# Kernel optimization log

Measured on AMD Instinct MI355X. Metric: run time of the kernel, lower is better.

The kernel has to match this reference:

```python
import jax, jax.numpy as jnp
from jax import lax
import numpy as np

B, N, NF, EF, MD = 16, 128, 9, 3, 5
H, D, FF, L, O = 24, 768, 3072, 12, 128
NA, NID, NOD, NE, NS, NED = 4608, 256, 256, 1536, 512, 128
S = N + 1
EPS = 1e-5


def setup_inputs() -> dict:
    key = jax.random.key(0)
    ks = iter(jax.random.split(key, 64))
    emb_s = 0.02
    lin_s = 0.02 / np.sqrt(L)

    def nrm(shape, s):
        return jax.random.normal(next(ks), shape, jnp.float32) * s

    inp = {
        'x': jax.random.randint(next(ks), (B, N, NF), 0, NA + 1),
        'in_degree': jax.random.randint(next(ks), (B, N), 0, NID),
        'out_degree': jax.random.randint(next(ks), (B, N), 0, NOD),
        'spatial_pos': jax.random.randint(next(ks), (B, N, N), 0, NS),
        'edge_input': jax.random.randint(next(ks), (B, N, N, MD, EF), 0, NE + 1),
        'attn_bias': jnp.zeros((B, S, S), jnp.float32),
        # embeddings (padding_idx=0 rows zeroed)
        'atom_emb': nrm((NA + 1, D), emb_s).at[0].set(0.0),
        'in_deg_emb': nrm((NID, D), emb_s).at[0].set(0.0),
        'out_deg_emb': nrm((NOD, D), emb_s).at[0].set(0.0),
        'graph_token': nrm((1, D), emb_s),
        'edge_emb': nrm((NE + 1, H), emb_s).at[0].set(0.0),
        'edge_dis_emb': nrm((NED, H, H), emb_s),
        'spatial_emb': nrm((NS, H), emb_s).at[0].set(0.0),
        'virt_dist': nrm((1, H), emb_s),
        # stacked per-layer params
        'ln1_g': jnp.ones((L, D)), 'ln1_b': jnp.zeros((L, D)),
        'wq': nrm((L, D, D), lin_s), 'bq': jnp.zeros((L, D)),
        'wk': nrm((L, D, D), lin_s), 'bk': jnp.zeros((L, D)),
        'wv': nrm((L, D, D), lin_s), 'bv': jnp.zeros((L, D)),
        'wo': nrm((L, D, D), lin_s), 'bo': jnp.zeros((L, D)),
        'ln2_g': jnp.ones((L, D)), 'ln2_b': jnp.zeros((L, D)),
        'w1': nrm((L, D, FF), lin_s), 'b1': jnp.zeros((L, FF)),
        'w2': nrm((L, FF, D), lin_s), 'b2': jnp.zeros((L, D)),
        'final_g': jnp.ones((D,)), 'final_b': jnp.zeros((D,)),
        'out_w': nrm((D, O), lin_s), 'out_b': jnp.zeros((O,)),
    }
    return inp


def _ln(v, g, b):
    m = v.mean(-1, keepdims=True)
    va = ((v - m) ** 2).mean(-1, keepdims=True)
    return (v - m) / jnp.sqrt(va + EPS) * g + b


def _forward(x, in_degree, out_degree, spatial_pos, edge_input, attn_bias,
             atom_emb, in_deg_emb, out_deg_emb, graph_token,
             edge_emb, edge_dis_emb, spatial_emb, virt_dist,
             ln1_g, ln1_b, wq, bq, wk, bk, wv, bv, wo, bo,
             ln2_g, ln2_b, w1, b1, w2, b2, final_g, final_b, out_w, out_b):
    nb = x.shape[0]
    # ---- graph attn bias ----
    # spatial bias [B,H,N,N]
    sp_bias = spatial_emb[spatial_pos].transpose(0, 3, 1, 2)
    # multi-hop edge bias
    sp_ = jnp.where(spatial_pos == 0, 1, spatial_pos)
    sp_ = jnp.where(sp_ > 1, sp_ - 1, sp_)
    sp_ = jnp.clip(sp_, 0, MD)
    ei = edge_emb[edge_input].mean(-2)                       # [B,N,N,MD,H]
    eo = jnp.einsum('bijdh,dhk->bijk', ei, edge_dis_emb[:MD])
    edge_bias = (eo / sp_[..., None].astype(jnp.float32)).transpose(0, 3, 1, 2)
    t = virt_dist.reshape(1, H, 1)                           # virtual-token distance
    gab = jnp.repeat(attn_bias[:, None], H, axis=1)          # [B,H,S,S]
    gab = gab.at[:, :, 1:, 1:].add(sp_bias + edge_bias)
    gab = gab.at[:, :, 1:, 0].add(t)
    gab = gab.at[:, :, 0, :].add(t)
    gab = gab + attn_bias[:, None]
    # ---- node features ----
    nf = atom_emb[x].sum(-2) + in_deg_emb[in_degree] + out_deg_emb[out_degree]
    h = jnp.concatenate([jnp.broadcast_to(graph_token[None], (nb, 1, D)), nf], axis=1)  # [B,S,D]
    dk = D // H
    scale = dk ** -0.5

    def step(hc, p):
        (g1, b1n, Wq, Bq, Wk, Bk, Wv, Bv, Wo, Bo, g2, b2n, W1, B1, W2, B2) = p
        y = _ln(hc, g1, b1n)
        q = (y @ Wq + Bq).reshape(nb, S, H, dk).transpose(0, 2, 1, 3) * scale
        k = (y @ Wk + Bk).reshape(nb, S, H, dk).transpose(0, 2, 1, 3)
        v = (y @ Wv + Bv).reshape(nb, S, H, dk).transpose(0, 2, 1, 3)
        att = jnp.einsum('bhqd,bhkd->bhqk', q, k) + gab
        att = jax.nn.softmax(att, axis=-1)
        ctx = jnp.einsum('bhqk,bhkd->bhqd', att, v)
        ctx = ctx.transpose(0, 2, 1, 3).reshape(nb, S, D)
        hc = hc + (ctx @ Wo + Bo)
        y = _ln(hc, g2, b2n)
        y = jax.nn.gelu(y @ W1 + B1, approximate=False) @ W2 + B2
        return hc + y, None

    h, _ = lax.scan(step, h, (ln1_g, ln1_b, wq, bq, wk, bk, wv, bv, wo, bo,
                              ln2_g, ln2_b, w1, b1, w2, b2))
    h = _ln(h, final_g, final_b)
    return h[:, 0] @ out_w + out_b  # [B,O]


def reference(x, in_degree, out_degree, spatial_pos, edge_input, attn_bias,
              atom_emb, in_deg_emb, out_deg_emb, graph_token,
              edge_emb, edge_dis_emb, spatial_emb, virt_dist,
              ln1_g, ln1_b, wq, bq, wk, bk, wv, bv, wo, bo,
              ln2_g, ln2_b, w1, b1, w2, b2, final_g, final_b, out_w, out_b):
    return _forward(x, in_degree, out_degree, spatial_pos, edge_input, attn_bias,
                    atom_emb, in_deg_emb, out_deg_emb, graph_token,
                    edge_emb, edge_dis_emb, spatial_emb, virt_dist,
                    ln1_g, ln1_b, wq, bq, wk, bk, wv, bv, wo, bo,
                    ln2_g, ln2_b, w1, b1, w2, b2, final_g, final_b, out_w, out_b)
```

## Files before the change

### kernel.cpp

```cpp
#include <hip/hip_runtime.h>
#include <hip/hip_bf16.h>
#include <math.h>

typedef __hip_bfloat16 bf16;
typedef __attribute__((ext_vector_type(8))) short short8;
typedef __attribute__((ext_vector_type(4))) short short4v;
typedef __attribute__((ext_vector_type(4))) float f32x4;

constexpr int NB = 16;
constexpr int ND = 128;
constexpr int SQ = 129;
constexpr int NH = 24;
constexpr int DM = 768;
constexpr int DF = 3072;
constexpr int NLAY = 12;
constexpr int MROWS = NB * SQ;
constexpr int DD2C = DM * DM;

__device__ __forceinline__ short f2bs(float f) {
  bf16 h = __float2bfloat16(f);
  return *(short*)&h;
}

__device__ __forceinline__ void gload16(const void* g, void* lds) {
  __builtin_amdgcn_global_load_lds(
      (const __attribute__((address_space(1))) unsigned int*)g,
      (__attribute__((address_space(3))) unsigned int*)lds, 16, 0, 0);
}

__global__ void k_nodefeat(const int* __restrict__ x, const int* __restrict__ ind,
                           const int* __restrict__ outd,
                           const float* __restrict__ atom, const float* __restrict__ ide,
                           const float* __restrict__ ode, const float* __restrict__ gtok,
                           float* __restrict__ h) {
  int bs = blockIdx.x;
  int b = bs / SQ, s = bs % SQ;
  int t = threadIdx.x;
  float* hrow = h + (size_t)bs * DM;
  if (s == 0) {
    for (int c = t; c < DM; c += 256) hrow[c] = gtok[c];
  } else {
    int n = s - 1;
    const int* xr = x + (b * ND + n) * 9;
    int a0 = xr[0], a1 = xr[1], a2 = xr[2], a3 = xr[3], a4 = xr[4];
    int a5 = xr[5], a6 = xr[6], a7 = xr[7], a8 = xr[8];
    int ii = ind[b * ND + n], oo = outd[b * ND + n];
    for (int c = t; c < DM; c += 256) {
      float acc = ide[(size_t)ii * DM + c] + ode[(size_t)oo * DM + c];
      acc += atom[(size_t)a0 * DM + c];
      acc += atom[(size_t)a1 * DM + c];
      acc += atom[(size_t)a2 * DM + c];
      acc += atom[(size_t)a3 * DM + c];
      acc += atom[(size_t)a4 * DM + c];
      acc += atom[(size_t)a5 * DM + c];
      acc += atom[(size_t)a6 * DM + c];
      acc += atom[(size_t)a7 * DM + c];
      acc += atom[(size_t)a8 * DM + c];
      hrow[c] = acc;
    }
  }
}

__global__ void k_gab_border(const float* __restrict__ ab, const float* __restrict__ virt,
                             float* __restrict__ gab) {
  int b = blockIdx.x;
  const int tot = NH * SQ + NH * ND;
  for (int idx = threadIdx.x; idx < tot; idx += 256) {
    if (idx < NH * SQ) {
      int hh = idx / SQ, j = idx % SQ;
      float v = 2.f * ab[((size_t)b * SQ + 0) * SQ + j] + virt[hh];
      gab[(((size_t)b * NH + hh) * SQ + 0) * SQ + j] = v;
    } else {
      int r = idx - NH * SQ;
      int hh = r / ND, i = r % ND + 1;
      float v = 2.f * ab[((size_t)b * SQ + i) * SQ + 0] + virt[hh];
      gab[(((size_t)b * NH + hh) * SQ + i) * SQ + 0] = v;
    }
  }
}

__global__ __launch_bounds__(256) void k_gab_edge(
    const int* __restrict__ spos, const int* __restrict__ eidx,
    const float* __restrict__ eemb, const float* __restrict__ edemb,
    const float* __restrict__ semb, const float* __restrict__ ab,
    float* __restrict__ gab) {
  __shared__ int eidxs[960];
  __shared__ short ei2[64 * 136];
  __shared__ short edT[32 * 136];
  __shared__ float ot[24][65];
  __shared__ float rinvA[64], a2A[64];
  __shared__ int spA[64];
  int bi = blockIdx.x;
  int half = bi & 1;
  int i = (bi >> 1) & 127;
  int b = bi >> 8;
  int j0 = half * 64;
  int t = threadIdx.x;
  const size_t rowbase = ((size_t)(b * ND + i)) * ND + j0;

  const int* esrc = eidx + rowbase * 15;
  for (int idx = t; idx < 960; idx += 256) eidxs[idx] = esrc[idx];
  for (int u = t; u < 720; u += 256) {
    int dh = u / 6, kq = u % 6;
    f32x4 v = *(const f32x4*)&edemb[dh * 24 + kq * 4];
    edT[(kq * 4 + 0) * 136 + dh] = f2bs(v[0]);
    edT[(kq * 4 + 1) * 136 + dh] = f2bs(v[1]);
    edT[(kq * 4 + 2) * 136 + dh] = f2bs(v[2]);
    edT[(kq * 4 + 3) * 136 + dh] = f2bs(v[3]);
  }
  for (int u = t; u < 1472; u += 256) {
    int k, dh;
    if (u < 384) { k = u >> 4; dh = 120 + (u & 15); }
    else { int v = u - 384; k = 24 + v / 136; dh = v % 136; }
    edT[k * 136 + dh] = 0;
  }
  if (t < 64) {
    int j = t;
    int sp = spos[rowbase + j];
    int spc = (sp == 0) ? 1 : sp;
    spc = (spc > 1) ? spc - 1 : spc;
    if (spc > 5) spc = 5;
    spA[j] = sp;
    rinvA[j] = 1.f / (float)spc;
    a2A[j] = 2.f * ab[((size_t)b * SQ + (i + 1)) * SQ + (j0 + j + 1)];
  }
  __syncthreads();

  {
    int j = t & 63, d = t >> 6;
#pragma unroll
    for (int pass = 0; pass < 2; pass++) {
      if (pass == 1) {
        if (t >= 64) break;
        j = t; d = 4;
      }
      const int* ep = &eidxs[j * 15 + d * 3];
      const float* r0 = eemb + (size_t)ep[0] * NH;
      const float* r1 = eemb + (size_t)ep[1] * NH;
      const float* r2 = eemb + (size_t)ep[2] * NH;
#pragma unroll
      for (int hq = 0; hq < 6; hq++) {
        f32x4 s = (*(const f32x4*)&r0[hq * 4] + *(const f32x4*)&r1[hq * 4] +
                   *(const f32x4*)&r2[hq * 4]) * (1.f / 3.f);
        short4v o;
        o[0] = f2bs(s[0]); o[1] = f2bs(s[1]); o[2] = f2bs(s[2]); o[3] = f2bs(s[3]);
        *(short4v*)&ei2[j * 136 + d * 24 + hq * 4] = o;
      }
    }
  }
  for (int idx = t; idx < 64 * 8; idx += 256) {
    int j = idx >> 3;
    ei2[j * 136 + 120 + (idx & 7)] = 0;
  }
  __syncthreads();

  int lane = t & 63, w = t >> 6;
  int fr = lane & 15, q = lane >> 4, fo = q * 8;
  f32x4 acc0 = {0.f, 0.f, 0.f, 0.f}, acc1 = {0.f, 0.f, 0.f, 0.f};
#pragma unroll
  for (int kk = 0; kk < 4; kk++) {
    short8 af = *(const short8*)&ei2[(w * 16 + fr) * 136 + kk * 32 + fo];
    short8 b0 = *(const short8*)&edT[(fr) * 136 + kk * 32 + fo];
    short8 b1 = *(const short8*)&edT[(16 + fr) * 136 + kk * 32 + fo];
    acc0 = __builtin_amdgcn_mfma_f32_16x16x32_bf16(af, b0, acc0, 0, 0, 0);
    acc1 = __builtin_amdgcn_mfma_f32_16x16x32_bf16(af, b1, acc1, 0, 0, 0);
  }
#pragma unroll
  for (int e = 0; e < 4; e++) {
    int j = w * 16 + q * 4 + e;
    ot[fr][j] = acc0[e];
    if (fr < 8) ot[16 + fr][j] = acc1[e];
  }
  __syncthreads();
  size_t obase = (((size_t)b * NH) * SQ + (i + 1)) * SQ + (j0 + 1);
  for (int idx = t; idx < 24 * 64; idx += 256) {
    int k = idx >> 6, j = idx & 63;
    float v = a2A[j] + semb[spA[j] * NH + k] + ot[k][j] * rinvA[j];
    gab[obase + (size_t)k * SQ * SQ + j] = v;
  }
}

struct Ptrs4 { const float* p[4]; };

template <int NW>
__global__ void k_transpose(Ptrs4 ps, short* __restrict__ dst, int R, int C,
                            size_t sstride) {
  __shared__ short tile[64][68];
  int z = blockIdx.z;
  const float* src = ps.p[z % NW] + (size_t)(z / NW) * sstride;
  short* d = dst + (size_t)z * (size_t)R * C;
  int r0 = blockIdx.x * 64, c0 = blockIdx.y * 64;
  int t = threadIdx.x;
  int tr = t >> 4, tc = (t & 15) * 4;
#pragma unroll
  for (int i = 0; i < 4; i++) {
    int r = tr + i * 16;
    f32x4 v = *(const f32x4*)(src + (size_t)(r0 + r) * C + c0 + tc);
    tile[r][tc + 0] = f2bs(v[0]);
    tile[r][tc + 1] = f2bs(v[1]);
    tile[r][tc + 2] = f2bs(v[2]);
    tile[r][tc + 3] = f2bs(v[3]);
  }
  __syncthreads();
#pragma unroll
  for (int i = 0; i < 4; i++) {
    int rr = tr + i * 16;
    short4v o;
    o[0] = tile[tc + 0][rr];
    o[1] = tile[tc + 1][rr];
    o[2] = tile[tc + 2][rr];
    o[3] = tile[tc + 3][rr];
    *(short4v*)(d + (size_t)(c0 + rr) * R + r0 + tc) = o;
  }
}

__global__ void k_ln(const float* __restrict__ h, const float* __restrict__ g,
                     const float* __restrict__ bb, bf16* __restrict__ y) {
  int r = blockIdx.x;
  int t = threadIdx.x, lane = t & 63, wid = t >> 6;
  __shared__ float red[8];
  const float* row = h + (size_t)r * DM;
  float v0 = row[t], v1 = row[t + 256], v2 = row[t + 512];
  float s = v0 + v1 + v2;
#pragma unroll
  for (int o = 32; o > 0; o >>= 1) s += __shfl_xor(s, o);
  if (lane == 0) red[wid] = s;
  __syncthreads();
  float mean = (red[0] + red[1] + red[2] + red[3]) * (1.f / 768.f);
  float d0 = v0 - mean, d1 = v1 - mean, d2 = v2 - mean;
  float q = d0 * d0 + d1 * d1 + d2 * d2;
#pragma unroll
  for (int o = 32; o > 0; o >>= 1) q += __shfl_xor(q, o);
  if (lane == 0) red[4 + wid] = q;
  __syncthreads();
  float var = (red[4] + red[5] + red[6] + red[7]) * (1.f / 768.f);
  float rstd = rsqrtf(var + 1e-5f);
  bf16* yr = y + (size_t)r * DM;
  yr[t] = __float2bfloat16(d0 * rstd * g[t] + bb[t]);
  yr[t + 256] = __float2bfloat16(d1 * rstd * g[t + 256] + bb[t + 256]);
  yr[t + 512] = __float2bfloat16(d2 * rstd * g[t + 512] + bb[t + 512]);
}

__global__ void k_ln_add2(float* __restrict__ h, const float* __restrict__ p0,
                          const float* __restrict__ p1, const float* __restrict__ cb,
                          const float* __restrict__ g, const float* __restrict__ bb,
                          bf16* __restrict__ y) {
  int r = blockIdx.x;
  int t = threadIdx.x, lane = t & 63, wid = t >> 6;
  __shared__ float red[8];
  size_t base = (size_t)r * DM;
  float v0 = h[base + t] + p0[base + t] + p1[base + t] + cb[t];
  float v1 = h[base + t + 256] + p0[base + t + 256] + p1[base + t + 256] + cb[t + 256];
  float v2 = h[base + t + 512] + p0[base + t + 512] + p1[base + t + 512] + cb[t + 512];
  h[base + t] = v0;
  h[base + t + 256] = v1;
  h[base + t + 512] = v2;
  float s = v0 + v1 + v2;
#pragma unroll
  for (int o = 32; o > 0; o >>= 1) s += __shfl_xor(s, o);
  if (lane == 0) red[wid] = s;
  __syncthreads();
  float mean = (red[0] + red[1] + red[2] + red[3]) * (1.f / 768.f);
  float d0 = v0 - mean, d1 = v1 - mean, d2 = v2 - mean;
  float q = d0 * d0 + d1 * d1 + d2 * d2;
#pragma unroll
  for (int o = 32; o > 0; o >>= 1) q += __shfl_xor(q, o);
  if (lane == 0) red[4 + wid] = q;
  __syncthreads();
  float var = (red[4] + red[5] + red[6] + red[7]) * (1.f / 768.f);
  float rstd = rsqrtf(var + 1e-5f);
  bf16* yr = y + base;
  yr[t] = __float2bfloat16(d0 * rstd * g[t] + bb[t]);
  yr[t + 256] = __float2bfloat16(d1 * rstd * g[t + 256] + bb[t + 256]);
  yr[t + 512] = __float2bfloat16(d2 * rstd * g[t + 512] + bb[t + 512]);
}

struct GemmPtrs {
  const short* bt[3];
  const float* bias[3];
  void* out[3];
  int aoff[3];
};

template <int MODE>
__device__ __forceinline__ void gemm_store(void* outp, size_t idx, float v) {
  if (MODE == 3) {
    ((float*)outp)[idx] = v;
  } else {
    float gg = 0.5f * v * (1.f + erff(v * 0.70710678118654752f));
    ((bf16*)outp)[idx] = __float2bfloat16(gg);
  }
}

template <int MODE>
__global__ __launch_bounds__(256, 3) void k_gemm128(const short* __restrict__ A, GemmPtrs p,
                                                    int M, int N, int K, int lda, int ldb) {
  __shared__ short At[128 * 64];
  __shared__ short Bt[128 * 64];
  int z = blockIdx.z;
  const short* BT = p.bt[z];
  const float* bias = p.bias[z];
  A += p.aoff[z];
  int m0 = blockIdx.x * 128, n0 = blockIdx.y * 128;
  int t = threadIdx.x, lane = t & 63, wid = t >> 6;
  int wr = wid >> 1, wc = wid & 1;
  f32x4 acc[4][4];
#pragma unroll
  for (int a = 0; a < 4; a++)
#pragma unroll
    for (int c = 0; c < 4; c++) acc[a][c] = (f32x4){0.f, 0.f, 0.f, 0.f};

  int lrow8 = lane >> 3;
  int lseg = (lane & 7) ^ lrow8;
  const short* gA[4];
  const short* gB[4];
#pragma unroll
  for (int i = 0; i < 4; i++) {
    int ar = m0 + wid * 32 + i * 8 + lrow8;
    if (ar >= M) ar = M - 1;
    gA[i] = A + (size_t)ar * lda + lseg * 8;
    int br = n0 + wid * 32 + i * 8 + lrow8;
    gB[i] = BT + (size_t)br * ldb + lseg * 8;
  }

  const int NIT = K >> 6;
  int fr = lane & 15, q = lane >> 4;
  for (int it = 0; it < NIT; ++it) {
    int k0 = it << 6;
#pragma unroll
    for (int i = 0; i < 4; i++) {
      gload16(gA[i] + k0, &At[(wid * 32 + i * 8) * 64]);
      gload16(gB[i] + k0, &Bt[(wid * 32 + i * 8) * 64]);
    }
    __syncthreads();
#pragma unroll
    for (int kk = 0; kk < 2; kk++) {
      int sg = ((q + kk * 4) ^ (fr & 7)) * 8;
      short8 af[4], bf[4];
#pragma unroll
      for (int mr = 0; mr < 4; mr++)
        af[mr] = *(const short8*)&At[(wr * 64 + mr * 16 + fr) * 64 + sg];
#pragma unroll
      for (int nc = 0; nc < 4; nc++)
        bf[nc] = *(const short8*)&Bt[(wc * 64 + nc * 16 + fr) * 64 + sg];
#pragma unroll
      for (int mr = 0; mr < 4; mr++)
#pragma unroll
        for (int nc = 0; nc < 4; nc++)
          acc[mr][nc] = __builtin_amdgcn_mfma_f32_16x16x32_bf16(af[mr], bf[nc], acc[mr][nc], 0, 0, 0);
    }
    __syncthreads();
  }

  int rsub = q * 4;
#pragma unroll
  for (int nc = 0; nc < 4; nc++) {
    int col = n0 + wc * 64 + nc * 16 + fr;
    float bv = (MODE == 3) ? 0.f : bias[col];
#pragma unroll
    for (int mr = 0; mr < 4; mr++) {
#pragma unroll
      for (int e = 0; e < 4; e++) {
        int r = m0 + wr * 64 + mr * 16 + rsub + e;
        if (r < M) gemm_store<MODE>(p.out[z], (size_t)r * N + col, acc[mr][nc][e] + bv);
      }
    }
  }
}

template <int MODE>
__global__ __launch_bounds__(256, 4) void k_gemm64(const short* __restrict__ A, GemmPtrs p,
                                                   int M, int N, int K, int lda, int ldb) {
  __shared__ short At[64 * 64];
  __shared__ short Bt[128 * 64];
  int z = blockIdx.z;
  const short* BT = p.bt[z];
  const float* bias = p.bias[z];
  A += p.aoff[z];
  int m0 = blockIdx.x * 64, n0 = blockIdx.y * 128;
  int t = threadIdx.x, lane = t & 63, wid = t >> 6;
  int wr = wid >> 1, wc = wid & 1;
  f32x4 acc[2][4];
#pragma unroll
  for (int a = 0; a < 2; a++)
#pragma unroll
    for (int c = 0; c < 4; c++) acc[a][c] = (f32x4){0.f, 0.f, 0.f, 0.f};

  int lrow8 = lane >> 3;
  int lseg = (lane & 7) ^ lrow8;
  const short* gA[2];
  const short* gB[4];
#pragma unroll
  for (int i = 0; i < 2; i++) {
    int ar = m0 + wid * 16 + i * 8 + lrow8;
    if (ar >= M) ar = M - 1;
    gA[i] = A + (size_t)ar * lda + lseg * 8;
  }
#pragma unroll
  for (int i = 0; i < 4; i++) {
    int br = n0 + wid * 32 + i * 8 + lrow8;
    gB[i] = BT + (size_t)br * ldb + lseg * 8;
  }

  const int NIT = K >> 6;
  int fr = lane & 15, q = lane >> 4;
  for (int it = 0; it < NIT; ++it) {
    int k0 = it << 6;
#pragma unroll
    for (int i = 0; i < 2; i++) gload16(gA[i] + k0, &At[(wid * 16 + i * 8) * 64]);
#pragma unroll
    for (int i = 0; i < 4; i++) gload16(gB[i] + k0, &Bt[(wid * 32 + i * 8) * 64]);
    __syncthreads();
#pragma unroll
    for (int kk = 0; kk < 2; kk++) {
      int sg = ((q + kk * 4) ^ (fr & 7)) * 8;
      short8 af[2], bf[4];
#pragma unroll
      for (int mr = 0; mr < 2; mr++)
        af[mr] = *(const short8*)&At[(wr * 32 + mr * 16 + fr) * 64 + sg];
#pragma unroll
      for (int nc = 0; nc < 4; nc++)
        bf[nc] = *(const short8*)&Bt[(wc * 64 + nc * 16 + fr) * 64 + sg];
#pragma unroll
      for (int mr = 0; mr < 2; mr++)
#pragma unroll
        for (int nc = 0; nc < 4; nc++)
          acc[mr][nc] = __builtin_amdgcn_mfma_f32_16x16x32_bf16(af[mr], bf[nc], acc[mr][nc], 0, 0, 0);
    }
    __syncthreads();
  }

  int rsub = q * 4;
#pragma unroll
  for (int nc = 0; nc < 4; nc++) {
    int col = n0 + wc * 64 + nc * 16 + fr;
    float bv = (MODE == 3) ? 0.f : bias[col];
#pragma unroll
    for (int mr = 0; mr < 2; mr++) {
#pragma unroll
      for (int e = 0; e < 4; e++) {
        int r = m0 + wr * 32 + mr * 16 + rsub + e;
        if (r < M) gemm_store<MODE>(p.out[z], (size_t)r * N + col, acc[mr][nc][e] + bv);
      }
    }
  }
}

__global__ __launch_bounds__(256) void k_fattn(const bf16* __restrict__ y,
                                               const short* __restrict__ wTl,
                                               const float* __restrict__ bq,
                                               const float* __restrict__ bk,
                                               const float* __restrict__ bv,
                                               const float* __restrict__ gab,
                                               bf16* __restrict__ ctx) {
  __shared__ short Ql[144 * 40];
  __shared__ short Kl[144 * 40];
  __shared__ short Vt[32 * 168];
  __shared__ short U[7680];
  __shared__ float bqa[32], bka[32], bva[32];
  short* Ay = U;
  short* Bw = U + 144 * 32;
  short* Pc = U;
  int bh = blockIdx.x;
  int b = bh / NH, hh = bh % NH;
  int t = threadIdx.x;
  int lane = t & 63, w = t >> 6;

  for (int idx = t; idx < 32 * 39; idx += 256) {
    int d = idx / 39, kk = 129 + (idx % 39);
    Vt[d * 168 + kk] = 0;
  }
  if (t < 32) {
    bqa[t] = bq[hh * 32 + t];
    bka[t] = bk[hh * 32 + t];
    bva[t] = bv[hh * 32 + t];
  }

  f32x4 acc[3][3][2];
#pragma unroll
  for (int i = 0; i < 3; i++)
#pragma unroll
    for (int m = 0; m < 3; m++)
#pragma unroll
      for (int nt = 0; nt < 2; nt++) acc[i][m][nt] = (f32x4){0.f, 0.f, 0.f, 0.f};

  int lr = lane >> 2;
  int lsg = (lane & 3) ^ (lr & 3);
  int fr = lane & 15, q = lane >> 4;
  const short* ybase = (const short*)y + (size_t)(b * SQ) * DM;

  for (int kt = 0; kt < 24; ++kt) {
    __syncthreads();
    for (int i = w; i < 9; i += 4) {
      int grow_ = i * 16 + lr;
      gload16(ybase + (size_t)grow_ * DM + kt * 32 + lsg * 8, &Ay[(i * 16) * 32]);
    }
    for (int i = w; i < 6; i += 4) {
      int m = i >> 1, half = i & 1;
      int nrow = hh * 32 + half * 16 + lr;
      gload16(wTl + (size_t)m * DD2C + (size_t)nrow * DM + kt * 32 + lsg * 8,
              &Bw[(m * 32 + half * 16) * 32]);
    }
    __syncthreads();
    int sg = (q ^ (fr & 3)) * 8;
#pragma unroll
    for (int i = 0; i < 3; i++) {
      int mt = w + 4 * i;
      if (mt > 8) break;
      short8 af = *(const short8*)&Ay[(mt * 16 + fr) * 32 + sg];
#pragma unroll
      for (int m = 0; m < 3; m++)
#pragma unroll
        for (int nt = 0; nt < 2; nt++) {
          short8 bf = *(const short8*)&Bw[(m * 32 + nt * 16 + fr) * 32 + sg];
          acc[i][m][nt] = __builtin_amdgcn_mfma_f32_16x16x32_bf16(af, bf, acc[i][m][nt], 0, 0, 0);
        }
    }
  }
  __syncthreads();
#pragma unroll
  for (int i = 0; i < 3; i++) {
    int mt = w + 4 * i;
    if (mt > 8) break;
#pragma unroll
    for (int nt = 0; nt < 2; nt++) {
      int coll = nt * 16 + fr;
      float bqv = bqa[coll], bkv = bka[coll], bvv = bva[coll];
#pragma unroll
      for (int e = 0; e < 4; e++) {
        int row = mt * 16 + q * 4 + e;
        Ql[row * 40 + coll] = f2bs(acc[i][0][nt][e] + bqv);
        Kl[row * 40 + coll] = f2bs(acc[i][1][nt][e] + bkv);
        if (row < 129) Vt[coll * 168 + row] = f2bs(acc[i][2][nt][e] + bvv);
      }
    }
  }
  __syncthreads();

  int c16 = lane & 15, q4 = lane >> 4;
  const float scale = 0.17677669529663689f;
  const float* gabp = gab + (((size_t)(b * NH + hh)) * SQ) * SQ;

  for (int mt = w; mt < 9; mt += 4) {
    f32x4 sc[9];
    short8 aq = *(const short8*)&Ql[(mt * 16 + c16) * 40 + q4 * 8];
#pragma unroll
    for (int nt = 0; nt < 9; nt++) {
      short8 bk8 = *(const short8*)&Kl[(nt * 16 + c16) * 40 + q4 * 8];
      f32x4 zz = {0.f, 0.f, 0.f, 0.f};
      sc[nt] = __builtin_amdgcn_mfma_f32_16x16x32_bf16(aq, bk8, zz, 0, 0, 0);
    }
#pragma unroll
    for (int e = 0; e < 4; e++) {
      int row = mt * 16 + q4 * 4 + e;
      int rr = row < 129 ? row : 128;
      const float* grow = gabp + (size_t)rr * SQ;
      float mloc = -1e30f;
#pragma unroll
      for (int nt = 0; nt < 9; nt++) {
        int col = nt * 16 + c16;
        float s = (col < 129) ? (sc[nt][e] * scale + grow[col]) : -1e30f;
        sc[nt][e] = s;
        mloc = fmaxf(mloc, s);
      }
#pragma unroll
      for (int o = 1; o < 16; o <<= 1) mloc = fmaxf(mloc, __shfl_xor(mloc, o));
      float sum = 0.f;
#pragma unroll
      for (int nt = 0; nt < 9; nt++) {
        float pp = __expf(sc[nt][e] - mloc);
        sc[nt][e] = pp;
        sum += pp;
      }
#pragma unroll
      for (int o = 1; o < 16; o <<= 1) sum += __shfl_xor(sum, o);
      float inv = 1.f / sum;
#pragma unroll
      for (int nt = 0; nt < 9; nt++) sc[nt][e] *= inv;
    }
    f32x4 oacc0 = {0.f, 0.f, 0.f, 0.f}, oacc1 = {0.f, 0.f, 0.f, 0.f};
#pragma unroll
    for (int c = 0; c < 5; c++) {
#pragma unroll
      for (int u = 0; u < 2; u++) {
        int nt = c * 2 + u;
        if (nt < 9) {
#pragma unroll
          for (int e = 0; e < 4; e++)
            Pc[(mt * 16 + q4 * 4 + e) * 40 + u * 16 + c16] = f2bs(sc[nt][e]);
        } else {
#pragma unroll
          for (int e = 0; e < 4; e++)
            Pc[(mt * 16 + q4 * 4 + e) * 40 + u * 16 + c16] = 0;
        }
      }
      asm volatile("s_waitcnt lgkmcnt(0)" ::: "memory");
      __builtin_amdgcn_sched_barrier(0);
      short8 ap = *(const short8*)&Pc[(mt * 16 + c16) * 40 + q4 * 8];
      short8 bv0 = *(const short8*)&Vt[(c16) * 168 + c * 32 + q4 * 8];
      short8 bv1 = *(const short8*)&Vt[(16 + c16) * 168 + c * 32 + q4 * 8];
      oacc0 = __builtin_amdgcn_mfma_f32_16x16x32_bf16(ap, bv0, oacc0, 0, 0, 0);
      oacc1 = __builtin_amdgcn_mfma_f32_16x16x32_bf16(ap, bv1, oacc1, 0, 0, 0);
    }
#pragma unroll
    for (int e = 0; e < 4; e++) {
      int row = mt * 16 + q4 * 4 + e;
      if (row < 129) {
        size_t obase = ((size_t)(b * SQ + row)) * DM + hh * 32;
        ctx[obase + c16] = __float2bfloat16(oacc0[e]);
        ctx[obase + 16 + c16] = __float2bfloat16(oacc1[e]);
      }
    }
  }
}

__global__ void k_final_add2(const float* __restrict__ h, const float* __restrict__ p0,
                             const float* __restrict__ p1, const float* __restrict__ cb,
                             const float* __restrict__ g, const float* __restrict__ bb,
                             const float* __restrict__ ow, const float* __restrict__ ob,
                             float* __restrict__ out) {
  int b = blockIdx.x;
  int t = threadIdx.x, lane = t & 63, wid = t >> 6;
  __shared__ float red[8];
  __shared__ float yn[768];
  size_t base = (size_t)(b * SQ) * DM;
  float v0 = h[base + t] + p0[base + t] + p1[base + t] + cb[t];
  float v1 = h[base + t + 256] + p0[base + t + 256] + p1[base + t + 256] + cb[t + 256];
  float v2 = h[base + t + 512] + p0[base + t + 512] + p1[base + t + 512] + cb[t + 512];
  float s = v0 + v1 + v2;
#pragma unroll
  for (int o = 32; o > 0; o >>= 1) s += __shfl_xor(s, o);
  if (lane == 0) red[wid] = s;
  __syncthreads();
  float mean = (red[0] + red[1] + red[2] + red[3]) * (1.f / 768.f);
  float d0 = v0 - mean, d1 = v1 - mean, d2 = v2 - mean;
  float q = d0 * d0 + d1 * d1 + d2 * d2;
#pragma unroll
  for (int o = 32; o > 0; o >>= 1) q += __shfl_xor(q, o);
  if (lane == 0) red[4 + wid] = q;
  __syncthreads();
  float var = (red[4] + red[5] + red[6] + red[7]) * (1.f / 768.f);
  float rstd = rsqrtf(var + 1e-5f);
  yn[t] = d0 * rstd * g[t] + bb[t];
  yn[t + 256] = d1 * rstd * g[t + 256] + bb[t + 256];
  yn[t + 512] = d2 * rstd * g[t + 512] + bb[t + 512];
  __syncthreads();
  if (t < 128) {
    float acc = ob[t];
    for (int d = 0; d < 768; d++) acc += yn[d] * ow[d * 128 + t];
    out[b * 128 + t] = acc;
  }
}

extern "C" void kernel_launch(void* const* d_in, const int* in_sizes, int n_in,
                              void* d_out, int out_size, void* d_ws, size_t ws_size,
                              hipStream_t stream) {
  (void)in_sizes; (void)n_in; (void)out_size;
  const int* x     = (const int*)d_in[0];
  const int* ind   = (const int*)d_in[1];
  const int* outd  = (const int*)d_in[2];
  const int* spos  = (const int*)d_in[3];
  const int* eidx  = (const int*)d_in[4];
  const float* ab   = (const float*)d_in[5];
  const float* atom = (const float*)d_in[6];
  const float* ide  = (const float*)d_in[7];
  const float* ode  = (const float*)d_in[8];
  const float* gtok = (const float*)d_in[9];
  const float* eemb = (const float*)d_in[10];
  const float* edemb= (const float*)d_in[11];
  const float* semb = (const float*)d_in[12];
  const float* virt = (const float*)d_in[13];
  const float* ln1g = (const float*)d_in[14];
  const float* ln1b = (const float*)d_in[15];
  const float* wq  = (const float*)d_in[16];
  const float* bq   = (const float*)d_in[17];
  const float* wk  = (const float*)d_in[18];
  const float* bk   = (const float*)d_in[19];
  const float* wv  = (const float*)d_in[20];
  const float* bv   = (const float*)d_in[21];
  const float* wo  = (const float*)d_in[22];
  const float* bo   = (const float*)d_in[23];
  const float* ln2g = (const float*)d_in[24];
  const float* ln2b = (const float*)d_in[25];
  const float* w1  = (const float*)d_in[26];
  const float* b1   = (const float*)d_in[27];
  const float* w2  = (const float*)d_in[28];
  const float* b2   = (const float*)d_in[29];
  const float* fg   = (const float*)d_in[30];
  const float* fb   = (const float*)d_in[31];
  const float* ow   = (const float*)d_in[32];
  const float* ob   = (const float*)d_in[33];
  float* out = (float*)d_out;

  const int DD2 = DM * DM;
  const size_t WQKVO = (size_t)DD2;
  const size_t WFF = (size_t)DM * DF;

  char* ws = (char*)d_ws;
  size_t off = 0;
  auto alloc = [&](size_t bytes) -> void* {
    void* p = ws + off;
    off += (bytes + 255) & ~(size_t)255;
    return p;
  };
  float* gab = (float*)alloc((size_t)NB * NH * SQ * SQ * 4);
  float* h   = (float*)alloc((size_t)MROWS * DM * 4);
  bf16* y    = (bf16*)alloc((size_t)MROWS * DM * 2);
  bf16* ctx  = (bf16*)alloc((size_t)MROWS * DM * 2);
  bf16* t1   = (bf16*)alloc((size_t)MROWS * DF * 2);
  float* p0  = (float*)alloc((size_t)MROWS * DM * 4);
  float* p1  = (float*)alloc((size_t)MROWS * DM * 4);

  size_t need_hoist = off + ((size_t)NLAY * 4 * WQKVO + 2 * (size_t)NLAY * WFF) * 2 + (1 << 20);
  bool hoist = ws_size >= need_hoist;
  short* wT  = (short*)alloc((hoist ? (size_t)NLAY * 4 * WQKVO : 4 * WQKVO) * 2);
  short* w1T = (short*)alloc((hoist ? (size_t)NLAY * WFF : WFF) * 2);
  short* w2T = (short*)alloc((hoist ? (size_t)NLAY * WFF : WFF) * 2);

  dim3 blk(256);
  k_nodefeat<<<dim3(NB * SQ), blk, 0, stream>>>(x, ind, outd, atom, ide, ode, gtok, h);
  k_gab_border<<<dim3(NB), blk, 0, stream>>>(ab, virt, gab);
  k_gab_edge<<<dim3(NB * ND * 2), blk, 0, stream>>>(spos, eidx, eemb, edemb, semb, ab, gab);

  if (hoist) {
    Ptrs4 pq; pq.p[0] = wq; pq.p[1] = wk; pq.p[2] = wv; pq.p[3] = wo;
    k_transpose<4><<<dim3(12, 12, 48), blk, 0, stream>>>(pq, wT, DM, DM, WQKVO);
    Ptrs4 pa; pa.p[0] = w1; pa.p[1] = pa.p[2] = pa.p[3] = w1;
    k_transpose<1><<<dim3(12, 48, 12), blk, 0, stream>>>(pa, w1T, DM, DF, WFF);
    Ptrs4 pb; pb.p[0] = w2; pb.p[1] = pb.p[2] = pb.p[3] = w2;
    k_transpose<1><<<dim3(48, 12, 12), blk, 0, stream>>>(pb, w2T, DF, DM, WFF);
  }

  for (int l = 0; l < NLAY; l++) {
    if (!hoist) {
      Ptrs4 pq;
      pq.p[0] = wq + (size_t)l * DD2; pq.p[1] = wk + (size_t)l * DD2;
      pq.p[2] = wv + (size_t)l * DD2; pq.p[3] = wo + (size_t)l * DD2;
      k_transpose<4><<<dim3(12, 12, 4), blk, 0, stream>>>(pq, wT, DM, DM, 0);
      Ptrs4 pa; pa.p[0] = w1 + (size_t)l * WFF; pa.p[1] = pa.p[2] = pa.p[3] = pa.p[0];
      k_transpose<1><<<dim3(12, 48, 1), blk, 0, stream>>>(pa, w1T, DM, DF, 0);
      Ptrs4 pb; pb.p[0] = w2 + (size_t)l * WFF; pb.p[1] = pb.p[2] = pb.p[3] = pb.p[0];
      k_transpose<1><<<dim3(48, 12, 1), blk, 0, stream>>>(pb, w2T, DF, DM, 0);
    }
    const short* wTl  = wT  + (hoist ? (size_t)l * 4 * WQKVO : 0);
    const short* w1Tl = w1T + (hoist ? (size_t)l * WFF : 0);
    const short* w2Tl = w2T + (hoist ? (size_t)l * WFF : 0);

    if (l == 0)
      k_ln<<<dim3(MROWS), blk, 0, stream>>>(h, ln1g, ln1b, y);

    k_fattn<<<dim3(NB * NH), blk, 0, stream>>>(y, wTl, bq + l * DM, bk + l * DM,
                                               bv + l * DM, gab, ctx);

    GemmPtrs go;
    go.bt[0] = wTl + 3 * DD2; go.bt[1] = wTl + 3 * DD2 + 384;
    go.bias[0] = go.bias[1] = nullptr;
    go.out[0] = p0; go.out[1] = p1;
    go.aoff[0] = 0; go.aoff[1] = 384;
    go.bt[2] = go.bt[0]; go.out[2] = p0; go.aoff[2] = 0; go.bias[2] = nullptr;
    k_gemm64<3><<<dim3(33, 6, 2), blk, 0, stream>>>((const short*)ctx, go, MROWS, DM, 384, DM, DM);

    k_ln_add2<<<dim3(MROWS), blk, 0, stream>>>(h, p0, p1, bo + l * DM,
                                               ln2g + l * DM, ln2b + l * DM, y);

    GemmPtrs g1;
    g1.bt[0] = g1.bt[1] = g1.bt[2] = w1Tl;
    g1.bias[0] = g1.bias[1] = g1.bias[2] = b1 + l * DF;
    g1.out[0] = g1.out[1] = g1.out[2] = t1;
    g1.aoff[0] = g1.aoff[1] = g1.aoff[2] = 0;
    k_gemm128<2><<<dim3(17, 24, 1), blk, 0, stream>>>((const short*)y, g1, MROWS, DF, DM, DM, DM);

    GemmPtrs g2;
    g2.bt[0] = w2Tl; g2.bt[1] = w2Tl + 1536;
    g2.bias[0] = g2.bias[1] = nullptr;
    g2.out[0] = p0; g2.out[1] = p1;
    g2.aoff[0] = 0; g2.aoff[1] = 1536;
    g2.bt[2] = g2.bt[0]; g2.out[2] = p0; g2.aoff[2] = 0; g2.bias[2] = nullptr;
    k_gemm64<3><<<dim3(33, 6, 2), blk, 0, stream>>>((const short*)t1, g2, MROWS, DM, 1536, DF, DF);

    if (l < NLAY - 1) {
      k_ln_add2<<<dim3(MROWS), blk, 0, stream>>>(h, p0, p1, b2 + l * DM,
                                                 ln1g + (l + 1) * DM, ln1b + (l + 1) * DM, y);
    } else {
      k_final_add2<<<dim3(NB), blk, 0, stream>>>(h, p0, p1, b2 + l * DM, fg, fb, ow, ob, out);
    }
  }
}
```

Before: 1.614 ms.

## Fuse node features with first LayerNorm, merge transposes, widen attention K-tile

Fuses the node-feature embedding sum, the first-layer LayerNorm and the attention-bias border writes into one kernel. This removes two launches and a round trip of h through memory. The three weight-transpose launches become a single flat-grid kernel. In the fused attention kernel the QKV projection now uses a 64-wide K step with an 8-way XOR swizzle instead of 32. That halves the loop iterations and barriers but doubles the shared staging buffer, which may lower occupancy.

```diff
diff --git a/kernel.cpp b/kernel.cpp
--- a/kernel.cpp
+++ b/kernel.cpp
@@ -28,24 +28,30 @@
       (__attribute__((address_space(3))) unsigned int*)lds, 16, 0, 0);
 }
 
-__global__ void k_nodefeat(const int* __restrict__ x, const int* __restrict__ ind,
-                           const int* __restrict__ outd,
-                           const float* __restrict__ atom, const float* __restrict__ ide,
-                           const float* __restrict__ ode, const float* __restrict__ gtok,
-                           float* __restrict__ h) {
+__global__ void k_nodefeat_ln(const int* __restrict__ x, const int* __restrict__ ind,
+                              const int* __restrict__ outd,
+                              const float* __restrict__ atom, const float* __restrict__ ide,
+                              const float* __restrict__ ode, const float* __restrict__ gtok,
+                              const float* __restrict__ ab, const float* __restrict__ virt,
+                              const float* __restrict__ g, const float* __restrict__ bb,
+                              float* __restrict__ h, bf16* __restrict__ y,
+                              float* __restrict__ gab) {
   int bs = blockIdx.x;
   int b = bs / SQ, s = bs % SQ;
-  int t = threadIdx.x;
-  float* hrow = h + (size_t)bs * DM;
+  int t = threadIdx.x, lane = t & 63, wid = t >> 6;
+  __shared__ float red[8];
+  float vv[3];
   if (s == 0) {
-    for (int c = t; c < DM; c += 256) hrow[c] = gtok[c];
+    vv[0] = gtok[t]; vv[1] = gtok[t + 256]; vv[2] = gtok[t + 512];
   } else {
     int n = s - 1;
     const int* xr = x + (b * ND + n) * 9;
     int a0 = xr[0], a1 = xr[1], a2 = xr[2], a3 = xr[3], a4 = xr[4];
     int a5 = xr[5], a6 = xr[6], a7 = xr[7], a8 = xr[8];
     int ii = ind[b * ND + n], oo = outd[b * ND + n];
-    for (int c = t; c < DM; c += 256) {
+#pragma unroll
+    for (int u = 0; u < 3; u++) {
+      int c = t + u * 256;
       float acc = ide[(size_t)ii * DM + c] + ode[(size_t)oo * DM + c];
       acc += atom[(size_t)a0 * DM + c];
       acc += atom[(size_t)a1 * DM + c];
@@ -56,25 +62,43 @@
       acc += atom[(size_t)a6 * DM + c];
       acc += atom[(size_t)a7 * DM + c];
       acc += atom[(size_t)a8 * DM + c];
-      hrow[c] = acc;
-    }
-  }
-}
-
-__global__ void k_gab_border(const float* __restrict__ ab, const float* __restrict__ virt,
-                             float* __restrict__ gab) {
-  int b = blockIdx.x;
-  const int tot = NH * SQ + NH * ND;
-  for (int idx = threadIdx.x; idx < tot; idx += 256) {
-    if (idx < NH * SQ) {
-      int hh = idx / SQ, j = idx % SQ;
-      float v = 2.f * ab[((size_t)b * SQ + 0) * SQ + j] + virt[hh];
-      gab[(((size_t)b * NH + hh) * SQ + 0) * SQ + j] = v;
-    } else {
-      int r = idx - NH * SQ;
-      int hh = r / ND, i = r % ND + 1;
-      float v = 2.f * ab[((size_t)b * SQ + i) * SQ + 0] + virt[hh];
-      gab[(((size_t)b * NH + hh) * SQ + i) * SQ + 0] = v;
+      vv[u] = acc;
+    }
+  }
+  float* hrow = h + (size_t)bs * DM;
+  hrow[t] = vv[0]; hrow[t + 256] = vv[1]; hrow[t + 512] = vv[2];
+  float sum = vv[0] + vv[1] + vv[2];
+#pragma unroll
+  for (int o = 32; o > 0; o >>= 1) sum += __shfl_xor(sum, o);
+  if (lane == 0) red[wid] = sum;
+  __syncthreads();
+  float mean = (red[0] + red[1] + red[2] + red[3]) * (1.f / 768.f);
+  float d0 = vv[0] - mean, d1 = vv[1] - mean, d2 = vv[2] - mean;
+  float q = d0 * d0 + d1 * d1 + d2 * d2;
+#pragma unroll
+  for (int o = 32; o > 0; o >>= 1) q += __shfl_xor(q, o);
+  if (lane == 0) red[4 + wid] = q;
+  __syncthreads();
+  float var = (red[4] + red[5] + red[6] + red[7]) * (1.f / 768.f);
+  float rstd = rsqrtf(var + 1e-5f);
+  bf16* yr = y + (size_t)bs * DM;
+  yr[t] = __float2bfloat16(d0 * rstd * g[t] + bb[t]);
+  yr[t + 256] = __float2bfloat16(d1 * rstd * g[t + 256] + bb[t + 256]);
+  yr[t + 512] = __float2bfloat16(d2 * rstd * g[t + 512] + bb[t + 512]);
+  if (bs < NB) {
+    int bb2 = bs;
+    const int tot = NH * SQ + NH * ND;
+    for (int idx = t; idx < tot; idx += 256) {
+      if (idx < NH * SQ) {
+        int hh = idx / SQ, j = idx % SQ;
+        float v = 2.f * ab[((size_t)bb2 * SQ + 0) * SQ + j] + virt[hh];
+        gab[(((size_t)bb2 * NH + hh) * SQ + 0) * SQ + j] = v;
+      } else {
+        int r = idx - NH * SQ;
+        int hh = r / ND, i = r % ND + 1;
+        float v = 2.f * ab[((size_t)bb2 * SQ + i) * SQ + 0] + virt[hh];
+        gab[(((size_t)bb2 * NH + hh) * SQ + i) * SQ + 0] = v;
+      }
     }
   }
 }
@@ -180,6 +204,62 @@
   }
 }
 
+struct TAll {
+  const float* wq; const float* wk; const float* wv; const float* wo;
+  const float* w1; const float* w2;
+  short* wT; short* w1T; short* w2T;
+};
+
+__global__ void k_transpose_all(TAll p) {
+  __shared__ short tile[64][68];
+  int id = blockIdx.x;
+  const float* src; short* d; int R, C, r0, c0;
+  if (id < 6912) {
+    int l = id / 576, rem = id % 576, mat = rem / 144, tl = rem % 144;
+    const float* srcs[4] = {p.wq, p.wk, p.wv, p.wo};
+    src = srcs[mat] + (size_t)l * DD2C;
+    d = p.wT + ((size_t)l * 4 + mat) * DD2C;
+    R = 768; C = 768;
+    r0 = (tl / 12) * 64; c0 = (tl % 12) * 64;
+  } else if (id < 13824) {
+    int id2 = id - 6912;
+    int l = id2 / 576, tl = id2 % 576;
+    src = p.w1 + (size_t)l * DM * DF;
+    d = p.w1T + (size_t)l * DM * DF;
+    R = 768; C = 3072;
+    r0 = (tl / 48) * 64; c0 = (tl % 48) * 64;
+  } else {
+    int id2 = id - 13824;
+    int l = id2 / 576, tl = id2 % 576;
+    src = p.w2 + (size_t)l * DM * DF;
+    d = p.w2T + (size_t)l * DM * DF;
+    R = 3072; C = 768;
+    r0 = (tl / 12) * 64; c0 = (tl % 12) * 64;
+  }
+  int t = threadIdx.x;
+  int tr = t >> 4, tc = (t & 15) * 4;
+#pragma unroll
+  for (int i = 0; i < 4; i++) {
+    int r = tr + i * 16;
+    f32x4 v = *(const f32x4*)(src + (size_t)(r0 + r) * C + c0 + tc);
+    tile[r][tc + 0] = f2bs(v[0]);
+    tile[r][tc + 1] = f2bs(v[1]);
+    tile[r][tc + 2] = f2bs(v[2]);
+    tile[r][tc + 3] = f2bs(v[3]);
+  }
+  __syncthreads();
+#pragma unroll
+  for (int i = 0; i < 4; i++) {
+    int rr = tr + i * 16;
+    short4v o;
+    o[0] = tile[tc + 0][rr];
+    o[1] = tile[tc + 1][rr];
+    o[2] = tile[tc + 2][rr];
+    o[3] = tile[tc + 3][rr];
+    *(short4v*)(d + (size_t)(c0 + rr) * R + r0 + tc) = o;
+  }
+}
+
 struct Ptrs4 { const float* p[4]; };
 
 template <int NW>
@@ -212,33 +292,6 @@
     o[3] = tile[tc + 3][rr];
     *(short4v*)(d + (size_t)(c0 + rr) * R + r0 + tc) = o;
   }
-}
-
-__global__ void k_ln(const float* __restrict__ h, const float* __restrict__ g,
-                     const float* __restrict__ bb, bf16* __restrict__ y) {
-  int r = blockIdx.x;
-  int t = threadIdx.x, lane = t & 63, wid = t >> 6;
-  __shared__ float red[8];
-  const float* row = h + (size_t)r * DM;
-  float v0 = row[t], v1 = row[t + 256], v2 = row[t + 512];
-  float s = v0 + v1 + v2;
-#pragma unroll
-  for (int o = 32; o > 0; o >>= 1) s += __shfl_xor(s, o);
-  if (lane == 0) red[wid] = s;
-  __syncthreads();
-  float mean = (red[0] + red[1] + red[2] + red[3]) * (1.f / 768.f);
-  float d0 = v0 - mean, d1 = v1 - mean, d2 = v2 - mean;
-  float q = d0 * d0 + d1 * d1 + d2 * d2;
-#pragma unroll
-  for (int o = 32; o > 0; o >>= 1) q += __shfl_xor(q, o);
-  if (lane == 0) red[4 + wid] = q;
-  __syncthreads();
-  float var = (red[4] + red[5] + red[6] + red[7]) * (1.f / 768.f);
-  float rstd = rsqrtf(var + 1e-5f);
-  bf16* yr = y + (size_t)r * DM;
-  yr[t] = __float2bfloat16(d0 * rstd * g[t] + bb[t]);
-  yr[t + 256] = __float2bfloat16(d1 * rstd * g[t + 256] + bb[t + 256]);
-  yr[t + 512] = __float2bfloat16(d2 * rstd * g[t + 512] + bb[t + 512]);
 }
 
 __global__ void k_ln_add2(float* __restrict__ h, const float* __restrict__ p0,
@@ -456,10 +509,10 @@
   __shared__ short Ql[144 * 40];
   __shared__ short Kl[144 * 40];
   __shared__ short Vt[32 * 168];
-  __shared__ short U[7680];
+  __shared__ short U[15360];
   __shared__ float bqa[32], bka[32], bva[32];
   short* Ay = U;
-  short* Bw = U + 144 * 32;
+  short* Bw = U + 9216;
   short* Pc = U;
   int bh = blockIdx.x;
   int b = bh / NH, hh = bh % NH;
@@ -484,37 +537,42 @@
 #pragma unroll
       for (int nt = 0; nt < 2; nt++) acc[i][m][nt] = (f32x4){0.f, 0.f, 0.f, 0.f};
 
-  int lr = lane >> 2;
-  int lsg = (lane & 3) ^ (lr & 3);
+  int lrow8 = lane >> 3;
+  int lseg8 = (lane & 7) ^ lrow8;
   int fr = lane & 15, q = lane >> 4;
   const short* ybase = (const short*)y + (size_t)(b * SQ) * DM;
 
-  for (int kt = 0; kt < 24; ++kt) {
+  for (int kt = 0; kt < 12; ++kt) {
+    int k0 = kt << 6;
     __syncthreads();
     for (int i = w; i < 9; i += 4) {
-      int grow_ = i * 16 + lr;
-      gload16(ybase + (size_t)grow_ * DM + kt * 32 + lsg * 8, &Ay[(i * 16) * 32]);
+      gload16(ybase + (size_t)(i * 16 + lrow8) * DM + k0 + lseg8 * 8, &Ay[(i * 16) * 64]);
+      gload16(ybase + (size_t)(i * 16 + 8 + lrow8) * DM + k0 + lseg8 * 8,
+              &Ay[(i * 16 + 8) * 64]);
     }
     for (int i = w; i < 6; i += 4) {
       int m = i >> 1, half = i & 1;
-      int nrow = hh * 32 + half * 16 + lr;
-      gload16(wTl + (size_t)m * DD2C + (size_t)nrow * DM + kt * 32 + lsg * 8,
-              &Bw[(m * 32 + half * 16) * 32]);
+      const short* wb = wTl + (size_t)m * DD2C + (size_t)(hh * 32 + half * 16) * DM + k0;
+      gload16(wb + (size_t)lrow8 * DM + lseg8 * 8, &Bw[(m * 32 + half * 16) * 64]);
+      gload16(wb + (size_t)(8 + lrow8) * DM + lseg8 * 8, &Bw[(m * 32 + half * 16 + 8) * 64]);
     }
     __syncthreads();
-    int sg = (q ^ (fr & 3)) * 8;
-#pragma unroll
-    for (int i = 0; i < 3; i++) {
-      int mt = w + 4 * i;
-      if (mt > 8) break;
-      short8 af = *(const short8*)&Ay[(mt * 16 + fr) * 32 + sg];
-#pragma unroll
-      for (int m = 0; m < 3; m++)
-#pragma unroll
-        for (int nt = 0; nt < 2; nt++) {
-          short8 bf = *(const short8*)&Bw[(m * 32 + nt * 16 + fr) * 32 + sg];
-          acc[i][m][nt] = __builtin_amdgcn_mfma_f32_16x16x32_bf16(af, bf, acc[i][m][nt], 0, 0, 0);
-        }
+#pragma unroll
+    for (int kk = 0; kk < 2; kk++) {
+      int sg = ((q + kk * 4) ^ (fr & 7)) * 8;
+#pragma unroll
+      for (int i = 0; i < 3; i++) {
+        int mt = w + 4 * i;
+        if (mt > 8) break;
+        short8 af = *(const short8*)&Ay[(mt * 16 + fr) * 64 + sg];
+#pragma unroll
+        for (int m = 0; m < 3; m++)
+#pragma unroll
+          for (int nt = 0; nt < 2; nt++) {
+            short8 bf = *(const short8*)&Bw[(m * 32 + nt * 16 + fr) * 64 + sg];
+            acc[i][m][nt] = __builtin_amdgcn_mfma_f32_16x16x32_bf16(af, bf, acc[i][m][nt], 0, 0, 0);
+          }
+      }
     }
   }
   __syncthreads();
@@ -718,17 +776,15 @@
   short* w2T = (short*)alloc((hoist ? (size_t)NLAY * WFF : WFF) * 2);
 
   dim3 blk(256);
-  k_nodefeat<<<dim3(NB * SQ), blk, 0, stream>>>(x, ind, outd, atom, ide, ode, gtok, h);
-  k_gab_border<<<dim3(NB), blk, 0, stream>>>(ab, virt, gab);
+  k_nodefeat_ln<<<dim3(MROWS), blk, 0, stream>>>(x, ind, outd, atom, ide, ode, gtok,
+                                                 ab, virt, ln1g, ln1b, h, y, gab);
   k_gab_edge<<<dim3(NB * ND * 2), blk, 0, stream>>>(spos, eidx, eemb, edemb, semb, ab, gab);
 
   if (hoist) {
-    Ptrs4 pq; pq.p[0] = wq; pq.p[1] = wk; pq.p[2] = wv; pq.p[3] = wo;
-    k_transpose<4><<<dim3(12, 12, 48), blk, 0, stream>>>(pq, wT, DM, DM, WQKVO);
-    Ptrs4 pa; pa.p[0] = w1; pa.p[1] = pa.p[2] = pa.p[3] = w1;
-    k_transpose<1><<<dim3(12, 48, 12), blk, 0, stream>>>(pa, w1T, DM, DF, WFF);
-    Ptrs4 pb; pb.p[0] = w2; pb.p[1] = pb.p[2] = pb.p[3] = w2;
-    k_transpose<1><<<dim3(48, 12, 12), blk, 0, stream>>>(pb, w2T, DF, DM, WFF);
+    TAll ta;
+    ta.wq = wq; ta.wk = wk; ta.wv = wv; ta.wo = wo; ta.w1 = w1; ta.w2 = w2;
+    ta.wT = wT; ta.w1T = w1T; ta.w2T = w2T;
+    k_transpose_all<<<dim3(20736), blk, 0, stream>>>(ta);
   }
 
   for (int l = 0; l < NLAY; l++) {
@@ -746,9 +802,6 @@
     const short* w1Tl = w1T + (hoist ? (size_t)l * WFF : 0);
     const short* w2Tl = w2T + (hoist ? (size_t)l * WFF : 0);
 
-    if (l == 0)
-      k_ln<<<dim3(MROWS), blk, 0, stream>>>(h, ln1g, ln1b, y);
-
     k_fattn<<<dim3(NB * NH), blk, 0, stream>>>(y, wTl, bq + l * DM, bk + l * DM,
                                                bv + l * DM, gab, ctx);
 
```

Measured after the change: 1.548 ms. 4.1% less time.
